# Performance work log

Hardware: AMD Instinct MI355X
Metric: run time of the kernel (lower is better)

## Reference

```python
import jax, jax.numpy as jnp
import numpy as np

B, T, C = 4, 2048, 1024


def setup_inputs() -> dict:
    key = jax.random.key(0)
    ks = jax.random.split(key, 5)
    s = 1.0 / np.sqrt(C)
    return {
        "X": jax.random.normal(ks[0], (B, T, C), dtype=jnp.float32),
        "Wq": jax.random.normal(ks[1], (C, C), dtype=jnp.float32) * s,
        "Wk": jax.random.normal(ks[2], (C, C), dtype=jnp.float32) * s,
        "Wv": jax.random.normal(ks[3], (C, C), dtype=jnp.float32) * s,
        "Wo": jax.random.normal(ks[4], (C, C), dtype=jnp.float32) * s,
    }


def reference(X, Wq, Wk, Wv, Wo):
    Bx, Tx, Cx = X.shape
    Q = X @ Wq  # [B,T,C]
    K = X @ Wk
    V = X @ Wv
    scores = jnp.einsum('btc,bsc->bts', Q, K) / jnp.sqrt(jnp.asarray(Cx, X.dtype))
    # causal mask: position t attends to s <= t
    causal = jnp.tril(jnp.ones((Tx, Tx), dtype=bool))
    scores = jnp.where(causal, scores, jnp.asarray(-jnp.inf, scores.dtype))
    weights = jax.nn.softmax(scores, axis=-1)
    out = jnp.einsum('bts,bsc->btc', weights, V)
    return out @ Wo
```

## Files before the change

### kernel.cpp

```cpp
#include <hip/hip_runtime.h>
#include <hip/hip_bf16.h>
#include <cmath>


typedef __attribute__((ext_vector_type(8))) __bf16 bf16x8;
typedef __attribute__((ext_vector_type(8))) short short8;
typedef __attribute__((ext_vector_type(4))) float f32x4;

__device__ __forceinline__ unsigned short f2bf(float f) {
  union { float f; unsigned u; } v; v.f = f;
  unsigned u = v.u;
  u += ((u >> 16) & 1u) + 0x7fffu;
  return (unsigned short)(u >> 16);
}
__device__ __forceinline__ float bf2f(unsigned short h) {
  union { unsigned u; float f; } v; v.u = ((unsigned)h) << 16;
  return v.f;
}

#define GLDS(gp, sp)                                                           \
  __builtin_amdgcn_global_load_lds(                                            \
      (const __attribute__((address_space(1))) void*)(gp),                     \
      (__attribute__((address_space(3))) void*)(sp), 16, 0, 0)

__global__ void cast_kernel(const float* __restrict__ src,
                            unsigned short* __restrict__ dst, int n) {
  int i = (blockIdx.x * blockDim.x + threadIdx.x) * 4;
  if (i >= n) return;
  float4 f = *(const float4*)(src + i);
  ushort4 o = make_ushort4(f2bf(f.x), f2bf(f.y), f2bf(f.z), f2bf(f.w));
  *(ushort4*)(dst + i) = o;
}

__global__ void transpose4(const float* __restrict__ w0,
                           const float* __restrict__ w1,
                           const float* __restrict__ w2,
                           const float* __restrict__ w3,
                           unsigned short* __restrict__ wcat,
                           unsigned short* __restrict__ wot,
                           int n) {
  const float* src = blockIdx.z == 0 ? w0 : blockIdx.z == 1 ? w1
                     : blockIdx.z == 2 ? w2 : w3;
  unsigned short* dst = blockIdx.z < 3 ? wcat + (size_t)blockIdx.z * n * n : wot;
  __shared__ float tile[32][33];
  int bx = blockIdx.x * 32, by = blockIdx.y * 32;
  int tx = threadIdx.x, ty = threadIdx.y;
#pragma unroll
  for (int i = 0; i < 32; i += 8)
    tile[ty + i][tx] = src[(size_t)(by + ty + i) * n + bx + tx];
  __syncthreads();
#pragma unroll
  for (int i = 0; i < 32; i += 8)
    dst[(size_t)(bx + ty + i) * n + by + tx] = f2bf(tile[tx][ty + i]);
}

template <typename OutT>
__global__ __launch_bounds__(256, 2)
void gemm_bt(const unsigned short* __restrict__ A, int lda, long long sA,
             const unsigned short* __restrict__ B, int ldb, long long sB,
             OutT* __restrict__ Cp, int ldc, long long sC,
             int K, float alpha, int tri, int kcap, int gx, int qkv) {
  A  += (long long)blockIdx.z * sA;
  B  += (long long)blockIdx.z * sB;
  Cp += (long long)blockIdx.z * sC;

  int by, bx;
  if (tri) {
    const int idx = blockIdx.x;
    by = (int)((sqrtf(8.f * idx + 1.f) - 1.f) * 0.5f);
    while (by * (by + 1) / 2 > idx) --by;
    while ((by + 1) * (by + 2) / 2 <= idx) ++by;
    bx = idx - by * (by + 1) / 2;
  } else if (gx > 0) {
    const int id = blockIdx.x;
    const int gs = gx * 8;
    const int g = id / gs, r = id - g * gs;
    bx = r >> 3;
    by = g * 8 + (r & 7);
  } else {
    by = blockIdx.y;
    bx = blockIdx.x;
  }
  const int m0 = by * 128;
  const int n0 = bx * 128;
  const int Keff = kcap ? min(K, m0 + 128) : K;

  const int tid  = threadIdx.x;
  const int lane = tid & 63;
  const int w    = tid >> 6;
  const int wm   = (w >> 1) * 64;
  const int wn   = (w & 1) * 64;
  const int quad = lane >> 4;
  const int l16  = lane & 15;

  __shared__ unsigned short As[128 * 64];
  __shared__ unsigned short Bs[128 * 64];

  f32x4 acc[4][4];
#pragma unroll
  for (int i = 0; i < 4; ++i)
#pragma unroll
    for (int j = 0; j < 4; ++j)
      acc[i][j] = (f32x4){0.f, 0.f, 0.f, 0.f};

  const int srow = tid >> 3;
  const int scol = ((tid & 7) ^ (srow & 7)) * 8;
  const unsigned short* gA = A + (long long)(m0 + srow) * lda + scol;
  const unsigned short* gB = B + (long long)(n0 + srow) * ldb + scol;
  const int rsw = l16 & 7;

  for (int kt = 0; kt < Keff; kt += 64) {
    __syncthreads();
#pragma unroll
    for (int r = 0; r < 4; ++r) {
      GLDS(gA + (long long)(r * 32) * lda + kt, As + r * 2048 + tid * 8);
      GLDS(gB + (long long)(r * 32) * ldb + kt, Bs + r * 2048 + tid * 8);
    }
    __syncthreads();
#pragma unroll
    for (int ks = 0; ks < 2; ++ks) {
      bf16x8 af[4], bfr[4];
#pragma unroll
      for (int i = 0; i < 4; ++i)
        af[i] = *(const bf16x8*)(As + (wm + i * 16 + l16) * 64 +
                                 ((ks * 4 + quad) ^ rsw) * 8);
#pragma unroll
      for (int j = 0; j < 4; ++j)
        bfr[j] = *(const bf16x8*)(Bs + (wn + j * 16 + l16) * 64 +
                                  ((ks * 4 + quad) ^ rsw) * 8);
#pragma unroll
      for (int i = 0; i < 4; ++i)
#pragma unroll
        for (int j = 0; j < 4; ++j)
          acc[i][j] = __builtin_amdgcn_mfma_f32_16x16x32_bf16(af[i], bfr[j],
                                                              acc[i][j], 0, 0, 0);
    }
  }

#pragma unroll
  for (int i = 0; i < 4; ++i) {
#pragma unroll
    for (int j = 0; j < 4; ++j) {
      const int row = m0 + wm + i * 16 + quad * 4;
      const int col = n0 + wn + j * 16 + l16;
      if constexpr (sizeof(OutT) == 2) {
        if (qkv) {
          if (col >= 2048) {
            const int b = row >> 11, t = row & 2047, cv = col - 2048;
            ushort4 o = make_ushort4(f2bf(acc[i][j][0]), f2bf(acc[i][j][1]),
                                     f2bf(acc[i][j][2]), f2bf(acc[i][j][3]));
            *(ushort4*)((unsigned short*)Cp + 16777216LL +
                        ((long long)(b * 1024 + cv)) * 2048 + t) = o;
          } else {
            unsigned short* dst =
                (unsigned short*)Cp + (col >= 1024 ? 8388608LL - 1024 : 0);
#pragma unroll
            for (int r = 0; r < 4; ++r)
              dst[(long long)(row + r) * 1024 + col] = f2bf(acc[i][j][r]);
          }
          continue;
        }
#pragma unroll
        for (int r = 0; r < 4; ++r)
          Cp[(long long)(row + r) * ldc + col] = (OutT)f2bf(acc[i][j][r] * alpha);
      } else {
#pragma unroll
        for (int r = 0; r < 4; ++r)
          Cp[(long long)(row + r) * ldc + col] = acc[i][j][r] * alpha;
      }
    }
  }
}

__global__ __launch_bounds__(256)
void softmax_causal(unsigned short* __restrict__ S, int T) {
  const long long row = blockIdx.x;
  const int t = (int)(row & (long long)(T - 1));
  const int limit = ((t >> 7) + 1) << 7;
  unsigned short* p = S + row * T;
  const int tid  = threadIdx.x;
  const int base = tid * 8;
  const bool active = base < limit;

  short8 raw = {};
  if (active) raw = *(const short8*)(p + base);
  float x[8];
  float mx = -1e30f;
#pragma unroll
  for (int j = 0; j < 8; ++j) {
    bool valid = active && (base + j) <= t;
    x[j] = valid ? bf2f((unsigned short)raw[j]) : -1e30f;
    mx = fmaxf(mx, x[j]);
  }
#pragma unroll
  for (int off = 32; off > 0; off >>= 1) mx = fmaxf(mx, __shfl_xor(mx, off));
  __shared__ float red[8];
  const int wv = tid >> 6;
  if ((tid & 63) == 0) red[wv] = mx;
  __syncthreads();
  mx = fmaxf(fmaxf(red[0], red[1]), fmaxf(red[2], red[3]));

  float sum = 0.f;
#pragma unroll
  for (int j = 0; j < 8; ++j) {
    bool valid = active && (base + j) <= t;
    x[j] = valid ? __expf(x[j] - mx) : 0.f;
    sum += x[j];
  }
#pragma unroll
  for (int off = 32; off > 0; off >>= 1) sum += __shfl_xor(sum, off);
  if ((tid & 63) == 0) red[4 + wv] = sum;
  __syncthreads();
  sum = red[4] + red[5] + red[6] + red[7];
  const float inv = 1.f / sum;

  if (active) {
    unsigned short out[8];
#pragma unroll
    for (int j = 0; j < 8; ++j) out[j] = f2bf(x[j] * inv);
    *(short8*)(p + base) = *(const short8*)out;
  }
}

extern "C" void kernel_launch(void* const* d_in, const int* in_sizes, int n_in,
                              void* d_out, int out_size, void* d_ws,
                              size_t ws_size, hipStream_t stream) {
  (void)in_sizes; (void)n_in; (void)out_size; (void)ws_size;
  const int Bb = 4, T = 2048, C = 1024;
  const int M = Bb * T;

  const float* X  = (const float*)d_in[0];
  const float* Wq = (const float*)d_in[1];
  const float* Wk = (const float*)d_in[2];
  const float* Wv = (const float*)d_in[3];
  const float* Wo = (const float*)d_in[4];
  float* Out = (float*)d_out;

  char* w = (char*)d_ws;
  unsigned short* Xb   = (unsigned short*)w; w += (size_t)M * C * 2;
  unsigned short* Wcat = (unsigned short*)w; w += (size_t)3 * C * C * 2;
  unsigned short* Wot  = (unsigned short*)w; w += (size_t)C * C * 2;
  unsigned short* Q    = (unsigned short*)w; w += (size_t)M * C * 2;
  unsigned short* Kb   = (unsigned short*)w; w += (size_t)M * C * 2;
  unsigned short* Vt   = (unsigned short*)w; w += (size_t)M * C * 2;
  unsigned short* O    = Xb;
  unsigned short* S    = (unsigned short*)d_out;

  cast_kernel<<<(M * C) / 4 / 256, 256, 0, stream>>>(X, Xb, M * C);
  transpose4<<<dim3(C / 32, C / 32, 4), dim3(32, 8), 0, stream>>>(
      Wq, Wk, Wv, Wo, Wcat, Wot, C);

  dim3 blk(256);
  gemm_bt<unsigned short><<<dim3((3 * C / 128) * (M / 128), 1, 1), blk, 0, stream>>>(
      Xb, C, 0, Wcat, C, 0, Q, C, 0, C, 1.f, 0, 0, 3 * C / 128, 1);
  const int ntri = (T / 128) * (T / 128 + 1) / 2;
  gemm_bt<unsigned short><<<dim3(ntri, 1, Bb), blk, 0, stream>>>(
      Q, C, (long long)T * C, Kb, C, (long long)T * C,
      S, T, (long long)T * T, C, 0.03125f, 1, 0, 0, 0);
  softmax_causal<<<M, 256, 0, stream>>>(S, T);
  gemm_bt<unsigned short><<<dim3((C / 128) * (T / 128), 1, Bb), blk, 0, stream>>>(
      S, T, (long long)T * T, Vt, T, (long long)C * T,
      O, C, (long long)T * C, T, 1.f, 0, 1, C / 128, 0);
  gemm_bt<float><<<dim3((C / 128) * (M / 128), 1, 1), blk, 0, stream>>>(
      O, C, 0, Wot, C, 0, Out, C, 0, C, 1.f, 0, 0, C / 128, 0);
}
```

Baseline: 274.9 us.

## Double-buffer LDS tiles in GEMM and reverse row order for causal PV

Adds a template parameter that selects double-buffered shared-memory staging for the GEMM kernel. The next K tile's async global-to-LDS load is issued before computing the current tile, which removes one barrier per iteration. It also reverses the row-block order for the causal-capped PV GEMM so the longest blocks launch first. LDS use doubles to 64KB per block, which may reduce occupancy, and the single barrier relies on async load completion semantics that could race.

```diff
diff --git a/kernel.cpp b/kernel.cpp
--- a/kernel.cpp
+++ b/kernel.cpp
@@ -54,7 +54,7 @@
     dst[(size_t)(bx + ty + i) * n + by + tx] = f2bf(tile[tx][ty + i]);
 }
 
-template <typename OutT>
+template <typename OutT, int NB>
 __global__ __launch_bounds__(256, 2)
 void gemm_bt(const unsigned short* __restrict__ A, int lda, long long sA,
              const unsigned short* __restrict__ B, int ldb, long long sB,
@@ -77,6 +77,7 @@
     const int g = id / gs, r = id - g * gs;
     bx = r >> 3;
     by = g * 8 + (r & 7);
+    if (kcap) by = (gridDim.x / gx) - 1 - by;
   } else {
     by = blockIdx.y;
     bx = blockIdx.x;
@@ -93,8 +94,8 @@
   const int quad = lane >> 4;
   const int l16  = lane & 15;
 
-  __shared__ unsigned short As[128 * 64];
-  __shared__ unsigned short Bs[128 * 64];
+  __shared__ unsigned short As[NB * 8192];
+  __shared__ unsigned short Bs[NB * 8192];
 
   f32x4 acc[4][4];
 #pragma unroll
@@ -109,24 +110,28 @@
   const unsigned short* gB = B + (long long)(n0 + srow) * ldb + scol;
   const int rsw = l16 & 7;
 
-  for (int kt = 0; kt < Keff; kt += 64) {
-    __syncthreads();
+  auto stage = [&](int kt, int buf) {
+    unsigned short* as = As + buf * 8192;
+    unsigned short* bs = Bs + buf * 8192;
 #pragma unroll
     for (int r = 0; r < 4; ++r) {
-      GLDS(gA + (long long)(r * 32) * lda + kt, As + r * 2048 + tid * 8);
-      GLDS(gB + (long long)(r * 32) * ldb + kt, Bs + r * 2048 + tid * 8);
-    }
-    __syncthreads();
+      GLDS(gA + (long long)(r * 32) * lda + kt, as + r * 2048 + tid * 8);
+      GLDS(gB + (long long)(r * 32) * ldb + kt, bs + r * 2048 + tid * 8);
+    }
+  };
+  auto compute = [&](int buf) {
+    const unsigned short* as = As + buf * 8192;
+    const unsigned short* bs = Bs + buf * 8192;
 #pragma unroll
     for (int ks = 0; ks < 2; ++ks) {
       bf16x8 af[4], bfr[4];
 #pragma unroll
       for (int i = 0; i < 4; ++i)
-        af[i] = *(const bf16x8*)(As + (wm + i * 16 + l16) * 64 +
+        af[i] = *(const bf16x8*)(as + (wm + i * 16 + l16) * 64 +
                                  ((ks * 4 + quad) ^ rsw) * 8);
 #pragma unroll
       for (int j = 0; j < 4; ++j)
-        bfr[j] = *(const bf16x8*)(Bs + (wn + j * 16 + l16) * 64 +
+        bfr[j] = *(const bf16x8*)(bs + (wn + j * 16 + l16) * 64 +
                                   ((ks * 4 + quad) ^ rsw) * 8);
 #pragma unroll
       for (int i = 0; i < 4; ++i)
@@ -134,6 +139,24 @@
         for (int j = 0; j < 4; ++j)
           acc[i][j] = __builtin_amdgcn_mfma_f32_16x16x32_bf16(af[i], bfr[j],
                                                               acc[i][j], 0, 0, 0);
+    }
+  };
+
+  if (NB == 2) {
+    stage(0, 0);
+    int cur = 0;
+    for (int kt = 0; kt < Keff; kt += 64) {
+      __syncthreads();
+      if (kt + 64 < Keff) stage(kt + 64, cur ^ 1);
+      compute(cur);
+      cur ^= 1;
+    }
+  } else {
+    for (int kt = 0; kt < Keff; kt += 64) {
+      __syncthreads();
+      stage(kt, 0);
+      __syncthreads();
+      compute(0);
     }
   }
 
@@ -251,16 +274,18 @@
       Wq, Wk, Wv, Wo, Wcat, Wot, C);
 
   dim3 blk(256);
-  gemm_bt<unsigned short><<<dim3((3 * C / 128) * (M / 128), 1, 1), blk, 0, stream>>>(
+  gemm_bt<unsigned short, 1><<<dim3((3 * C / 128) * (M / 128), 1, 1), blk, 0,
+                               stream>>>(
       Xb, C, 0, Wcat, C, 0, Q, C, 0, C, 1.f, 0, 0, 3 * C / 128, 1);
   const int ntri = (T / 128) * (T / 128 + 1) / 2;
-  gemm_bt<unsigned short><<<dim3(ntri, 1, Bb), blk, 0, stream>>>(
+  gemm_bt<unsigned short, 2><<<dim3(ntri, 1, Bb), blk, 0, stream>>>(
       Q, C, (long long)T * C, Kb, C, (long long)T * C,
       S, T, (long long)T * T, C, 0.03125f, 1, 0, 0, 0);
   softmax_causal<<<M, 256, 0, stream>>>(S, T);
-  gemm_bt<unsigned short><<<dim3((C / 128) * (T / 128), 1, Bb), blk, 0, stream>>>(
+  gemm_bt<unsigned short, 2><<<dim3((C / 128) * (T / 128), 1, Bb), blk, 0,
+                               stream>>>(
       S, T, (long long)T * T, Vt, T, (long long)C * T,
       O, C, (long long)T * C, T, 1.f, 0, 1, C / 128, 0);
-  gemm_bt<float><<<dim3((C / 128) * (M / 128), 1, 1), blk, 0, stream>>>(
+  gemm_bt<float, 2><<<dim3((C / 128) * (M / 128), 1, 1), blk, 0, stream>>>(
       O, C, 0, Wot, C, 0, Out, C, 0, C, 1.f, 0, 0, C / 128, 0);
 }
```

After: 279.3 us. About the same (+1.6%).
